# Kernel tuning notes

Measured on AMD Instinct MI355X. Metric: run time of the kernel, lower is better.

## Reference

```python
import jax, jax.numpy as jnp
import numpy as np

S, B, IN = 8, 8192, 2      # obs seq_len, batch, input_size
E, H, OUT, PRED = 256, 1024, 2, 12  # embed, rnn_size, output_size, pred_len


def setup_inputs() -> dict:
    key = jax.random.key(0)
    ks = jax.random.split(key, 20)
    w = lambda k, shape, fan: (jax.random.normal(k, shape, jnp.float32) / np.sqrt(fan))
    return {
        "obs_traj": jax.random.normal(ks[0], (S, B, IN), jnp.float32),
        # input embedding Linear(IN -> E)
        "W_emb": w(ks[1], (E, IN), IN), "b_emb": jnp.zeros((E,), jnp.float32),
        # LSTM layer 0: input E -> H  (torch gate order i,f,g,o)
        "W_ih0": w(ks[2], (4 * H, E), E), "W_hh0": w(ks[3], (4 * H, H), H),
        "b_ih0": jnp.zeros((4 * H,), jnp.float32), "b_hh0": jnp.zeros((4 * H,), jnp.float32),
        # LSTM layer 1: input H -> H
        "W_ih1": w(ks[4], (4 * H, H), H), "W_hh1": w(ks[5], (4 * H, H), H),
        "b_ih1": jnp.zeros((4 * H,), jnp.float32), "b_hh1": jnp.zeros((4 * H,), jnp.float32),
        # output_seq MLP: H -> 32 -> 16 -> OUT
        "W1": w(ks[6], (32, H), H), "b1": jnp.zeros((32,), jnp.float32),
        "W2": w(ks[7], (16, 32), 32), "b2": jnp.zeros((16,), jnp.float32),
        "W3": w(ks[8], (OUT, 16), 16), "b3": jnp.zeros((OUT,), jnp.float32),
    }


def reference(obs_traj, W_emb, b_emb, W_ih0, W_hh0, b_ih0, b_hh0,
              W_ih1, W_hh1, b_ih1, b_hh1, W1, b1, W2, b2, W3, b3):
    # Dropout layers are identity in eval mode.
    def embed(x):
        return jax.nn.relu(x @ W_emb.T + b_emb)

    def cell(x, h, c, Wih, Whh, bih, bhh):
        g = x @ Wih.T + h @ Whh.T + (bih + bhh)          # [B, 4H]
        i, f, gg, o = jnp.split(g, 4, axis=-1)
        c = jax.nn.sigmoid(f) * c + jax.nn.sigmoid(i) * jnp.tanh(gg)
        h = jax.nn.sigmoid(o) * jnp.tanh(c)
        return h, c

    def lstm_step(hc, x):
        h0, c0, h1, c1 = hc
        h0, c0 = cell(x, h0, c0, W_ih0, W_hh0, b_ih0, b_hh0)
        h1, c1 = cell(h0, h1, c1, W_ih1, W_hh1, b_ih1, b_hh1)
        return (h0, c0, h1, c1), h1

    def mlp(h):
        h = jax.nn.relu(h @ W1.T + b1)
        h = jax.nn.relu(h @ W2.T + b2)
        return h @ W3.T + b3

    z = jnp.zeros((B, H), obs_traj.dtype)
    hc = (z, z, z, z)

    # --- encoding: run LSTM over the observed trajectory ---
    emb_obs = embed(obs_traj)                             # [S, B, E]
    hc, _ = jax.lax.scan(lambda c, x: lstm_step(c, x), hc, emb_obs)

    curr = obs_traj[-1]                                   # [B, IN]
    curr_emb = embed(curr)

    def dec_step(carry, _):
        hc, curr, curr_emb = carry
        hc, out = lstm_step(hc, curr_emb)                 # out: [B, H]
        nxt = curr + mlp(out)                             # displacement decode
        return (hc, nxt, embed(nxt)), nxt

    _, preds = jax.lax.scan(dec_step, (hc, curr, curr_emb), None, length=PRED)
    return preds                                          # [PRED, B, OUT]
```

## Files before the change

kernel.cpp:

```cpp
#include <hip/hip_runtime.h>
#include <hip/hip_bf16.h>
#include <stdint.h>

typedef __hip_bfloat16 bf16;
typedef __attribute__((ext_vector_type(8))) short bf16x8;
typedef __attribute__((ext_vector_type(4))) float f32x4;
typedef __attribute__((ext_vector_type(8))) unsigned short us8;

#define NB 8192
#define NE 256
#define NH 1024

__device__ __forceinline__ float bf2f(unsigned short u) {
  union { unsigned int i; float f; } x; x.i = ((unsigned int)u) << 16; return x.f;
}
__device__ __forceinline__ float sigm(float x) {
  return __builtin_amdgcn_rcpf(1.f + __expf(-x));
}
__device__ __forceinline__ float tanh_f(float x) {
  return 1.f - 2.f * __builtin_amdgcn_rcpf(1.f + __expf(2.f * x));
}

#define BAR() __builtin_amdgcn_s_barrier()
#define LGKM0() do { asm volatile("s_waitcnt lgkmcnt(0)" ::: "memory"); \
                     __builtin_amdgcn_sched_barrier(0); } while (0)
#define VMW(N) asm volatile("s_waitcnt vmcnt(" #N ")" ::: "memory")

#define MFMA32(MH)                                                            \
  do {                                                                        \
    __builtin_amdgcn_s_setprio(1);                                            \
    _Pragma("unroll") for (int i_ = 0; i_ < 4; ++i_)                          \
      _Pragma("unroll") for (int g_ = 0; g_ < 4; ++g_) {                      \
        acc[(MH)*4 + i_][g_] = __builtin_amdgcn_mfma_f32_16x16x32_bf16(       \
            af[i_], bv[g_], acc[(MH)*4 + i_][g_], 0, 0, 0);                   \
        acc[(MH)*4 + i_][g_] = __builtin_amdgcn_mfma_f32_16x16x32_bf16(       \
            af[4 + i_], bv[4 + g_], acc[(MH)*4 + i_][g_], 0, 0, 0);           \
      }                                                                       \
    __builtin_amdgcn_s_setprio(0);                                            \
  } while (0)

#define LDA8(BUF, MH)                                                         \
  do {                                                                        \
    const char* Ab_ = (const char*)&As[BUF][0][0];                            \
    _Pragma("unroll") for (int i_ = 0; i_ < 4; ++i_) {                        \
      int ro_ = (wr * 128 + (MH)*64 + i_ * 16 + l15) * 128;                   \
      af[i_]     = *(const bf16x8*)(Ab_ + ro_ + co0);                         \
      af[4 + i_] = *(const bf16x8*)(Ab_ + ro_ + co1);                         \
    }                                                                         \
  } while (0)

#define LDB8(BUF)                                                             \
  do {                                                                        \
    const char* Bb_ = (const char*)&Bs[BUF][0][0];                            \
    _Pragma("unroll") for (int g_ = 0; g_ < 4; ++g_) {                        \
      int ro_ = (g_ * 64 + nc * 16 + l15) * 128;                              \
      bv[g_]     = *(const bf16x8*)(Bb_ + ro_ + co0);                         \
      bv[4 + g_] = *(const bf16x8*)(Bb_ + ro_ + co1);                         \
    }                                                                         \
  } while (0)

__global__ __launch_bounds__(512, 2) void k_cell(
    const bf16* __restrict__ X, int ldx, int Kx,
    const bf16* __restrict__ Hin, int Kh,
    const bf16* __restrict__ Wih, const bf16* __restrict__ Whh,
    const float* __restrict__ bias, float* __restrict__ Cst,
    bf16* __restrict__ Hout, int czero)
{
  __shared__ bf16 As[2][256][64];
  __shared__ bf16 Bs[2][256][64];

  const int tid = threadIdx.x;
  const int l = tid & 63;
  const int l15 = l & 15;
  const int wv = tid >> 6;
  const int wr = wv >> 2;
  const int nc = wv & 3;

  const int bid = blockIdx.x;
  const int xcd = bid & 7, j = bid >> 3;
  const int m0 = (xcd * 4 + (j & 3)) * 256;
  const int hc0 = (j >> 2) * 64;

  const int NT = (Kx + Kh) >> 6;
  const int T = NT >> 1;

  const int rowid = tid >> 3;
  const int ch = (tid & 7) ^ (rowid & 7);
  const int wv8 = wv * 8;

  const int co0 = (((l >> 4) + 0) ^ (l & 7)) * 16;
  const int co1 = (((l >> 4) + 4) ^ (l & 7)) * 16;

  f32x4 acc[8][4];
  f32x4 zero4 = {0.f, 0.f, 0.f, 0.f};
#pragma unroll
  for (int i = 0; i < 8; ++i)
#pragma unroll
    for (int j2 = 0; j2 < 4; ++j2) acc[i][j2] = zero4;

  auto stage_a = [&](int buf, int half, int kt) {
    int kc = kt << 6;
    const bf16* src; size_t ld;
    if (kc < Kx) { src = X + kc; ld = (size_t)ldx; }
    else         { src = Hin + (kc - Kx); ld = NH; }
#pragma unroll
    for (int rnd = 0; rnd < 2; ++rnd) {
      int tr = rnd * 128 + half * 64;
      const bf16* gp = src + (size_t)(m0 + tr + rowid) * ld + ch * 8;
      __builtin_amdgcn_global_load_lds(
          (const __attribute__((address_space(1))) void*)gp,
          (__attribute__((address_space(3))) void*)&As[buf][tr + wv8][0],
          16, 0, 0);
    }
  };
  auto stage_b = [&](int buf, int half, int kt) {
    int kc = kt << 6;
    const bf16* src; size_t ld;
    if (kc < Kx) { src = Wih + kc; ld = (size_t)Kx; }
    else         { src = Whh + (kc - Kx); ld = NH; }
#pragma unroll
    for (int rnd = 0; rnd < 2; ++rnd) {
      int gate = rnd * 2 + half;
      const bf16* gp = src + (size_t)(gate * NH + hc0 + rowid) * ld + ch * 8;
      __builtin_amdgcn_global_load_lds(
          (const __attribute__((address_space(1))) void*)gp,
          (__attribute__((address_space(3))) void*)&Bs[buf][gate * 64 + wv8][0],
          16, 0, 0);
    }
  };

  stage_a(0, 0, 0);
  stage_a(0, 1, 0);
  stage_b(0, 0, 0);
  stage_b(0, 1, 0);
  stage_a(1, 0, 1);
  VMW(2);
  BAR();

  for (int t = 0; t < T; ++t) {
    const int kt1 = 2 * t + 1;
    const bool last = (t == T - 1);
    bf16x8 af[8], bv[8];

    LDB8(0); LDA8(0, 0);
    stage_a(1, 1, kt1);
    stage_b(1, 0, kt1);
    stage_b(1, 1, kt1);
    BAR(); LGKM0();
    MFMA32(0);
    BAR();

    LDA8(0, 1);
    if (!last) stage_a(0, 0, kt1 + 1);
    BAR(); LGKM0();
    MFMA32(1);
    if (last) { VMW(0); } else { VMW(2); }
    BAR();

    LDB8(1); LDA8(1, 0);
    if (!last) {
      stage_a(0, 1, kt1 + 1);
      stage_b(0, 0, kt1 + 1);
      stage_b(0, 1, kt1 + 1);
    }
    BAR(); LGKM0();
    MFMA32(0);
    BAR();

    LDA8(1, 1);
    if (!last) stage_a(1, 0, kt1 + 2);
    BAR(); LGKM0();
    MFMA32(1);
    if (!last) { VMW(2); }
    BAR();
  }

  const int ecol = hc0 + nc * 16 + l15;
  const float bi = bias[ecol];
  const float bff = bias[NH + ecol];
  const float bg = bias[2 * NH + ecol];
  const float bo = bias[3 * NH + ecol];
  const int r0 = m0 + wr * 128 + ((l >> 4) << 2);
#pragma unroll
  for (int m = 0; m < 8; ++m) {
#pragma unroll
    for (int r = 0; r < 4; ++r) {
      int row = r0 + m * 16 + r;
      size_t idx = (size_t)row * NH + ecol;
      float gi = sigm(acc[m][0][r] + bi);
      float gf = sigm(acc[m][1][r] + bff);
      float gg = tanh_f(acc[m][2][r] + bg);
      float go = sigm(acc[m][3][r] + bo);
      float cold = czero ? 0.f : Cst[idx];
      float cn = gf * cold + gi * gg;
      Cst[idx] = cn;
      Hout[idx] = __float2bfloat16(go * tanh_f(cn));
    }
  }
}

__global__ __launch_bounds__(256) void k_mlp(
    const bf16* __restrict__ h1, const bf16* __restrict__ W1b, const float* __restrict__ b1,
    const float* __restrict__ W2, const float* __restrict__ b2,
    const float* __restrict__ W3, const float* __restrict__ b3,
    const float* __restrict__ cin, float* __restrict__ cout,
    float* __restrict__ preds, const float* __restrict__ Wemb,
    const float* __restrict__ bemb, bf16* __restrict__ embout)
{
  const int l = threadIdx.x & 63;
  const int row = blockIdx.x * 4 + (threadIdx.x >> 6);

  const us8* hp = (const us8*)(h1 + (size_t)row * NH + l * 16);
  us8 hv0 = hp[0], hv1 = hp[1];
  float h[16];
#pragma unroll
  for (int j = 0; j < 8; ++j) { h[j] = bf2f(hv0[j]); h[8 + j] = bf2f(hv1[j]); }

  float y1[32];
#pragma unroll
  for (int j = 0; j < 32; ++j) {
    const us8* wp = (const us8*)(W1b + (size_t)j * NH + l * 16);
    us8 w0 = wp[0], w1 = wp[1];
    float d = 0.f;
#pragma unroll
    for (int k = 0; k < 8; ++k) {
      d = fmaf(h[k], bf2f(w0[k]), d);
      d = fmaf(h[8 + k], bf2f(w1[k]), d);
    }
#pragma unroll
    for (int off2 = 32; off2 > 0; off2 >>= 1) d += __shfl_xor(d, off2);
    y1[j] = fmaxf(d + b1[j], 0.f);
  }

  float y2[16];
#pragma unroll
  for (int m = 0; m < 16; ++m) {
    float s = b2[m];
#pragma unroll
    for (int j = 0; j < 32; ++j) s = fmaf(W2[m * 32 + j], y1[j], s);
    y2[m] = fmaxf(s, 0.f);
  }
  float o0 = b3[0], o1 = b3[1];
#pragma unroll
  for (int k = 0; k < 16; ++k) {
    o0 = fmaf(W3[k], y2[k], o0);
    o1 = fmaf(W3[16 + k], y2[k], o1);
  }
  float n0 = cin[row * 2] + o0;
  float n1 = cin[row * 2 + 1] + o1;
  if (l == 0) {
    preds[row * 2] = n0; preds[row * 2 + 1] = n1;
    cout[row * 2] = n0;  cout[row * 2 + 1] = n1;
  }
#pragma unroll
  for (int q = 0; q < 4; ++q) {
    int e = l + q * 64;
    float v = fmaf(n0, Wemb[e * 2], fmaf(n1, Wemb[e * 2 + 1], bemb[e]));
    embout[(size_t)row * NE + e] = __float2bfloat16(fmaxf(v, 0.f));
  }
}

__global__ void k_embed(const float* __restrict__ x, const float* __restrict__ W,
                        const float* __restrict__ b, bf16* __restrict__ out) {
  const int l = threadIdx.x & 63;
  const int row = (blockIdx.x * 256 + threadIdx.x) >> 6;
  float x0 = x[row * 2], x1 = x[row * 2 + 1];
#pragma unroll
  for (int q = 0; q < 4; ++q) {
    int e = l + q * 64;
    float v = fmaf(x0, W[e * 2], fmaf(x1, W[e * 2 + 1], b[e]));
    out[(size_t)row * NE + e] = __float2bfloat16(fmaxf(v, 0.f));
  }
}

__global__ void k_f2b(const float* __restrict__ in, bf16* __restrict__ out, int n) {
  int i = (blockIdx.x * 256 + threadIdx.x) * 4;
  if (i >= n) return;
  float4 v = *(const float4*)(in + i);
  out[i] = __float2bfloat16(v.x);
  out[i + 1] = __float2bfloat16(v.y);
  out[i + 2] = __float2bfloat16(v.z);
  out[i + 3] = __float2bfloat16(v.w);
}

__global__ void k_badd(const float* __restrict__ a, const float* __restrict__ b,
                       float* __restrict__ o, int n) {
  int i = blockIdx.x * 256 + threadIdx.x;
  if (i < n) o[i] = a[i] + b[i];
}

extern "C" void kernel_launch(void* const* d_in, const int* in_sizes, int n_in,
                              void* d_out, int out_size, void* d_ws, size_t ws_size,
                              hipStream_t stream) {
  const float* obs   = (const float*)d_in[0];
  const float* Wemb  = (const float*)d_in[1];
  const float* bemb  = (const float*)d_in[2];
  const float* Wih0f = (const float*)d_in[3];
  const float* Whh0f = (const float*)d_in[4];
  const float* bih0  = (const float*)d_in[5];
  const float* bhh0  = (const float*)d_in[6];
  const float* Wih1f = (const float*)d_in[7];
  const float* Whh1f = (const float*)d_in[8];
  const float* bih1  = (const float*)d_in[9];
  const float* bhh1  = (const float*)d_in[10];
  const float* W1f   = (const float*)d_in[11];
  const float* b1m   = (const float*)d_in[12];
  const float* W2    = (const float*)d_in[13];
  const float* b2    = (const float*)d_in[14];
  const float* W3    = (const float*)d_in[15];
  const float* b3    = (const float*)d_in[16];

  char* ws = (char*)d_ws;
  size_t off = 0;
  auto alloc = [&](size_t bytes) -> void* {
    void* p = ws + off;
    off += (bytes + 255) & ~(size_t)255;
    return p;
  };
  bf16* wih0 = (bf16*)alloc((size_t)4096 * 256 * 2);
  bf16* whh0 = (bf16*)alloc((size_t)4096 * 1024 * 2);
  bf16* wih1 = (bf16*)alloc((size_t)4096 * 1024 * 2);
  bf16* whh1 = (bf16*)alloc((size_t)4096 * 1024 * 2);
  bf16* w1b  = (bf16*)alloc((size_t)32 * 1024 * 2);
  float* b0c = (float*)alloc((size_t)4096 * 4);
  float* b1c = (float*)alloc((size_t)4096 * 4);
  bf16* emb  = (bf16*)alloc((size_t)8 * NB * NE * 2);
  bf16* h0a  = (bf16*)alloc((size_t)NB * NH * 2);
  bf16* h0b  = (bf16*)alloc((size_t)NB * NH * 2);
  bf16* h1a  = (bf16*)alloc((size_t)NB * NH * 2);
  bf16* h1b  = (bf16*)alloc((size_t)NB * NH * 2);
  float* c0  = (float*)alloc((size_t)NB * NH * 4);
  float* c1  = (float*)alloc((size_t)NB * NH * 4);
  float* curr = (float*)alloc((size_t)NB * 2 * 4);
  bf16* cemb = (bf16*)alloc((size_t)NB * NE * 2);

  k_f2b<<<1024, 256, 0, stream>>>(Wih0f, wih0, 4096 * 256);
  k_f2b<<<4096, 256, 0, stream>>>(Whh0f, whh0, 4096 * 1024);
  k_f2b<<<4096, 256, 0, stream>>>(Wih1f, wih1, 4096 * 1024);
  k_f2b<<<4096, 256, 0, stream>>>(Whh1f, whh1, 4096 * 1024);
  k_f2b<<<32, 256, 0, stream>>>(W1f, w1b, 32 * 1024);
  k_badd<<<16, 256, 0, stream>>>(bih0, bhh0, b0c, 4096);
  k_badd<<<16, 256, 0, stream>>>(bih1, bhh1, b1c, 4096);
  k_embed<<<(8 * NB) / 4, 256, 0, stream>>>(obs, Wemb, bemb, emb);

  bf16* h0buf[2] = {h0a, h0b};
  bf16* h1buf[2] = {h1a, h1b};
  float* preds = (float*)d_out;

  for (int t = 0; t < 20; ++t) {
    const bf16* xin;
    if (t < 8)       xin = emb + (size_t)t * NB * NE;
    else if (t == 8) xin = emb + (size_t)7 * NB * NE;
    else             xin = cemb;
    int cu = t & 1, pv = cu ^ 1;
    int kh = (t == 0) ? 0 : NH;
    k_cell<<<512, 512, 0, stream>>>(xin, NE, NE, h0buf[pv], kh,
                                    wih0, whh0, b0c, c0, h0buf[cu], t == 0);
    k_cell<<<512, 512, 0, stream>>>(h0buf[cu], NH, NH, h1buf[pv], kh,
                                    wih1, whh1, b1c, c1, h1buf[cu], t == 0);
    if (t >= 8) {
      int p = t - 8;
      const float* cin = (p == 0) ? (obs + (size_t)7 * NB * 2) : curr;
      k_mlp<<<NB / 4, 256, 0, stream>>>(h1buf[cu], w1b, b1m, W2, b2, W3, b3,
                                        cin, curr, preds + (size_t)p * NB * 2,
                                        Wemb, bemb, cemb);
    }
  }
}
```

Measured before the change: 5.001 ms.

## Add 4-stage K=32 pipelined cell kernel for layer-1 LSTM GEMM

Adds a new LSTM cell kernel, k_cell6, that uses a four-buffer LDS ring with 32-wide K tiles. It keeps three stages of loads in flight and interleaves next-tile LDS reads with the MFMA chain through sched_group_barrier. Layer 1, where K=2048 dominates, now uses this kernel, while layer 0 keeps the original kernel under the name k_cell3. The aim is to hide global-load latency better and overlap LDS reads with MFMAs, at the cost of more barriers per K and different occupancy, since launch_bounds no longer requests 2 blocks per CU.

```diff
diff --git a/kernel.cpp b/kernel.cpp
--- a/kernel.cpp
+++ b/kernel.cpp
@@ -25,6 +25,12 @@
 #define LGKM0() do { asm volatile("s_waitcnt lgkmcnt(0)" ::: "memory"); \
                      __builtin_amdgcn_sched_barrier(0); } while (0)
 #define VMW(N) asm volatile("s_waitcnt vmcnt(" #N ")" ::: "memory")
+
+#define GLDS(G, S)                                                            \
+  __builtin_amdgcn_global_load_lds(                                           \
+      (const __attribute__((address_space(1))) void*)(G),                     \
+      (__attribute__((address_space(3))) void*)(S), 16, 0, 0)
+
 
 #define MFMA32(MH)                                                            \
   do {                                                                        \
@@ -59,7 +65,7 @@
     }                                                                         \
   } while (0)
 
-__global__ __launch_bounds__(512, 2) void k_cell(
+__global__ __launch_bounds__(512, 2) void k_cell3(
     const bf16* __restrict__ X, int ldx, int Kx,
     const bf16* __restrict__ Hin, int Kh,
     const bf16* __restrict__ Wih, const bf16* __restrict__ Whh,
@@ -107,10 +113,7 @@
     for (int rnd = 0; rnd < 2; ++rnd) {
       int tr = rnd * 128 + half * 64;
       const bf16* gp = src + (size_t)(m0 + tr + rowid) * ld + ch * 8;
-      __builtin_amdgcn_global_load_lds(
-          (const __attribute__((address_space(1))) void*)gp,
-          (__attribute__((address_space(3))) void*)&As[buf][tr + wv8][0],
-          16, 0, 0);
+      GLDS(gp, &As[buf][tr + wv8][0]);
     }
   };
   auto stage_b = [&](int buf, int half, int kt) {
@@ -122,10 +125,7 @@
     for (int rnd = 0; rnd < 2; ++rnd) {
       int gate = rnd * 2 + half;
       const bf16* gp = src + (size_t)(gate * NH + hc0 + rowid) * ld + ch * 8;
-      __builtin_amdgcn_global_load_lds(
-          (const __attribute__((address_space(1))) void*)gp,
-          (__attribute__((address_space(3))) void*)&Bs[buf][gate * 64 + wv8][0],
-          16, 0, 0);
+      GLDS(gp, &Bs[buf][gate * 64 + wv8][0]);
     }
   };
 
@@ -174,6 +174,150 @@
     if (!last) { VMW(2); }
     BAR();
   }
+
+  const int ecol = hc0 + nc * 16 + l15;
+  const float bi = bias[ecol];
+  const float bff = bias[NH + ecol];
+  const float bg = bias[2 * NH + ecol];
+  const float bo = bias[3 * NH + ecol];
+  const int r0 = m0 + wr * 128 + ((l >> 4) << 2);
+#pragma unroll
+  for (int m = 0; m < 8; ++m) {
+#pragma unroll
+    for (int r = 0; r < 4; ++r) {
+      int row = r0 + m * 16 + r;
+      size_t idx = (size_t)row * NH + ecol;
+      float gi = sigm(acc[m][0][r] + bi);
+      float gf = sigm(acc[m][1][r] + bff);
+      float gg = tanh_f(acc[m][2][r] + bg);
+      float go = sigm(acc[m][3][r] + bo);
+      float cold = czero ? 0.f : Cst[idx];
+      float cn = gf * cold + gi * gg;
+      Cst[idx] = cn;
+      Hout[idx] = __float2bfloat16(go * tanh_f(cn));
+    }
+  }
+}
+
+
+#define MM6(M, G)                                                             \
+  acc[M][G] = __builtin_amdgcn_mfma_f32_16x16x32_bf16(af[M], bv[G], acc[M][G], 0, 0, 0)
+
+#define LDAF(N)                                                               \
+  do { _Pragma("unroll") for (int m_ = 0; m_ < 8; ++m_)                       \
+    af[m_] = *(const bf16x8*)(Aarena + base_a + ((N)*16384 + m_ * 1024));     \
+  } while (0)
+#define LDBV(N)                                                               \
+  do { _Pragma("unroll") for (int g_ = 0; g_ < 4; ++g_)                       \
+    bv[g_] = *(const bf16x8*)(Barena + base_b + ((N)*16384 + g_ * 4096));     \
+  } while (0)
+
+#define REGION(KT, CUR, NXT, STG, DOSTAGE, DOTRAIL, VKIND)                    \
+  do {                                                                        \
+    if (DOSTAGE) stage(STG, (KT) + 3);                                        \
+    if ((VKIND) == 1) { VMW(4); }                                             \
+    if ((VKIND) == 2) { VMW(0); }                                             \
+    LGKM0();                                                                  \
+    __builtin_amdgcn_s_setprio(1);                                            \
+    _Pragma("unroll")                                                         \
+    for (int m_ = 0; m_ < 8; ++m_) {                                          \
+      MM6(m_, 0); MM6(m_, 1); MM6(m_, 2); MM6(m_, 3);                         \
+      if (DOTRAIL) {                                                          \
+        af[m_] = *(const bf16x8*)(Aarena + base_a + ((NXT)*16384 + m_ * 1024)); \
+        __builtin_amdgcn_sched_group_barrier(0x8, 4, 0);                      \
+        __builtin_amdgcn_sched_group_barrier(0x100, 1, 0);                    \
+      }                                                                       \
+    }                                                                         \
+    __builtin_amdgcn_s_setprio(0);                                            \
+    if (DOTRAIL) { LDBV(NXT); }                                               \
+    BAR();                                                                    \
+  } while (0)
+
+__global__ __launch_bounds__(512) void k_cell6(
+    const bf16* __restrict__ X, int ldx, int Kx,
+    const bf16* __restrict__ Hin, int Kh,
+    const bf16* __restrict__ Wih, const bf16* __restrict__ Whh,
+    const float* __restrict__ bias, float* __restrict__ Cst,
+    bf16* __restrict__ Hout, int czero)
+{
+  __shared__ bf16 As[4][256][32];
+  __shared__ bf16 Bs[4][256][32];
+
+  const int tid = threadIdx.x;
+  const int l = tid & 63;
+  const int l15 = l & 15;
+  const int wv = tid >> 6;
+  const int wr = wv >> 2;
+  const int nc = wv & 3;
+
+  const int bid = blockIdx.x;
+  const int xcd = bid & 7, jj = bid >> 3;
+  const int m0 = (xcd * 4 + (jj & 3)) * 256;
+  const int hc0 = (jj >> 2) * 64;
+
+  const int NT32 = (Kx + Kh) >> 5;
+
+  const int ra0 = tid >> 2;
+  const int sch = (tid & 3) ^ ((tid >> 3) & 3);
+  const bf16* pAx = X + (size_t)(m0 + ra0) * ldx + sch * 8;
+  const bf16* pAh = Hin + (size_t)(m0 + ra0) * NH + sch * 8;
+  const size_t rAx2 = (size_t)128 * ldx, rAh2 = (size_t)128 * NH;
+  const int grow0 = (ra0 >> 6) * NH + hc0 + (ra0 & 63);
+  const bf16* pBx = Wih + (size_t)grow0 * Kx + sch * 8;
+  const bf16* pBh = Whh + (size_t)grow0 * NH + sch * 8;
+  const size_t rBx2 = (size_t)2 * NH * Kx, rBh2 = (size_t)2 * NH * NH;
+
+  char* Aarena = (char*)&As[0][0][0];
+  char* Barena = (char*)&Bs[0][0][0];
+
+  const int chp = (l >> 4) ^ ((l15 >> 1) & 3);
+  const int base_a = (wr * 128 + l15) * 64 + chp * 16;
+  const int base_b = (nc * 16 + l15) * 64 + chp * 16;
+
+  f32x4 acc[8][4];
+  f32x4 zero4 = {0.f, 0.f, 0.f, 0.f};
+#pragma unroll
+  for (int i = 0; i < 8; ++i)
+#pragma unroll
+    for (int j2 = 0; j2 < 4; ++j2) acc[i][j2] = zero4;
+
+  auto stage = [&](int buf, int kt) {
+    int kc = kt << 5;
+    char* da = Aarena + buf * 16384 + tid * 16;
+    char* db = Barena + buf * 16384 + tid * 16;
+    if (kc < Kx) {
+      const bf16* a0 = pAx + kc;
+      GLDS(a0, da); GLDS(a0 + rAx2, da + 8192);
+      const bf16* b0 = pBx + kc;
+      GLDS(b0, db); GLDS(b0 + rBx2, db + 8192);
+    } else {
+      const bf16* a0 = pAh + (kc - Kx);
+      GLDS(a0, da); GLDS(a0 + rAh2, da + 8192);
+      const bf16* b0 = pBh + (kc - Kx);
+      GLDS(b0, db); GLDS(b0 + rBh2, db + 8192);
+    }
+  };
+
+  bf16x8 af[8], bv[4];
+
+  stage(0, 0);
+  stage(1, 1);
+  stage(2, 2);
+  VMW(4);
+  BAR();
+  LDAF(0); LDBV(0);
+
+  int kt = 0;
+  for (; kt < NT32 - 4; kt += 4) {
+    REGION(kt + 0, 0, 1, 3, 1, 1, 1);
+    REGION(kt + 1, 1, 2, 0, 1, 1, 1);
+    REGION(kt + 2, 2, 3, 1, 1, 1, 1);
+    REGION(kt + 3, 3, 0, 2, 1, 1, 1);
+  }
+  REGION(kt + 0, 0, 1, 3, 1, 1, 1);
+  REGION(kt + 1, 1, 2, 0, 0, 1, 2);
+  REGION(kt + 2, 2, 3, 0, 0, 1, 0);
+  REGION(kt + 3, 3, 0, 0, 0, 0, 0);
 
   const int ecol = hc0 + nc * 16 + l15;
   const float bi = bias[ecol];
@@ -354,10 +498,10 @@
     else             xin = cemb;
     int cu = t & 1, pv = cu ^ 1;
     int kh = (t == 0) ? 0 : NH;
-    k_cell<<<512, 512, 0, stream>>>(xin, NE, NE, h0buf[pv], kh,
-                                    wih0, whh0, b0c, c0, h0buf[cu], t == 0);
-    k_cell<<<512, 512, 0, stream>>>(h0buf[cu], NH, NH, h1buf[pv], kh,
-                                    wih1, whh1, b1c, c1, h1buf[cu], t == 0);
+    k_cell3<<<512, 512, 0, stream>>>(xin, NE, NE, h0buf[pv], kh,
+                                     wih0, whh0, b0c, c0, h0buf[cu], t == 0);
+    k_cell6<<<512, 512, 0, stream>>>(h0buf[cu], NH, NH, h1buf[pv], kh,
+                                     wih1, whh1, b1c, c1, h1buf[cu], t == 0);
     if (t >= 8) {
       int p = t - 8;
       const float* cin = (p == 0) ? (obs + (size_t)7 * NB * 2) : curr;
```

New measurement: 6.614 ms. 1.32x slower.
